# Optimization experiments

Measured on AMD Instinct MI355X. Metric: run time of the kernel, lower is better.

The kernel has to match this reference:

```python
import jax, jax.numpy as jnp
import numpy as np

B, T, QD, CD = 64, 1024, 1024, 512  # batch, encoder steps, query_dim, context_dim


def setup_inputs() -> dict:
    key = jax.random.key(0)
    k1, k2, k3, k4 = jax.random.split(key, 4)
    query = jax.random.normal(k1, (B, 1, QD), dtype=jnp.float32)
    inputs = jax.random.normal(k2, (B, T, CD), dtype=jnp.float32)
    # init_states: alpha = [1, 1e-7, 1e-7, ...], u = 0.5, sq = 1.4
    alpha = jnp.concatenate([jnp.ones((B, 1)), jnp.full((B, T - 1), 1e-7)], axis=1).astype(jnp.float32)
    u = jnp.full((B, 1), 0.5, dtype=jnp.float32)
    sq = jnp.full((B, 1), 1.4, dtype=jnp.float32)
    W_u = (jax.random.normal(k3, (QD + CD, 1)) * 0.02).astype(jnp.float32)
    b_u = jnp.zeros((1,), dtype=jnp.float32)
    W_sq = (jax.random.normal(k4, (QD + CD, 1)) * 0.02).astype(jnp.float32)
    b_sq = jnp.zeros((1,), dtype=jnp.float32)
    return {"query": query, "inputs": inputs, "alpha": alpha, "u": u, "sq": sq,
            "W_u": W_u, "b_u": b_u, "W_sq": W_sq, "b_sq": b_sq}


def reference(query, inputs, alpha, u, sq, W_u, b_u, W_sq, b_sq):
    # shift alpha forward by one step (pad a zero at position 0)
    fwd_shifted = jnp.pad(alpha[:, :-1], ((0, 0), (1, 0)))            # [B, T]
    a = ((1.0 - u) * alpha + u * fwd_shifted + 1e-6) ** sq           # [B, T]
    a = a / jnp.sum(a, axis=1, keepdims=True)                        # normalized alpha
    context = jnp.einsum('bt,btc->bc', a, inputs)                    # [B, CD]
    ta_input = jnp.concatenate([context, query[:, 0, :]], axis=-1)   # [B, CD+QD]
    u_new = jax.nn.sigmoid(ta_input @ W_u + b_u)                     # [B, 1]
    sq_new = jax.nn.sigmoid(ta_input @ W_sq + b_sq) + 1.0            # [B, 1] (dynamicsq)
    return context, a, u_new, sq_new
```

## Files before the change

kernel.cpp:

```cpp
#include <hip/hip_runtime.h>
#include <math.h>

#define B_  64
#define T_  1024
#define QD_ 1024
#define CD_ 512

__global__ __launch_bounds__(256) void attn_alpha_kernel(
    const float* __restrict__ alpha, const float* __restrict__ u,
    const float* __restrict__ sq, float* __restrict__ out_a)
{
    const int b   = blockIdx.x;
    const int tid = threadIdx.x;
    __shared__ float s_alpha[T_];
    __shared__ float s_red[4];

    ((float4*)s_alpha)[tid] = ((const float4*)(alpha + (size_t)b * T_))[tid];
    __syncthreads();

    const float ub  = u[b];
    const float sqb = sq[b];
    const float omu = 1.0f - ub;

    const int t0 = tid * 4;
    float raw[4];
    float lsum = 0.f;
#pragma unroll
    for (int i = 0; i < 4; ++i) {
        const int t = t0 + i;
        const float prev = (t == 0) ? 0.f : s_alpha[t - 1];
        const float x = omu * s_alpha[t] + ub * prev + 1e-6f;
        const float r = powf(x, sqb);
        raw[i] = r;
        lsum += r;
    }
#pragma unroll
    for (int off = 32; off > 0; off >>= 1) lsum += __shfl_down(lsum, off);
    if ((tid & 63) == 0) s_red[tid >> 6] = lsum;
    __syncthreads();
    if (tid == 0) s_red[0] = s_red[0] + s_red[1] + s_red[2] + s_red[3];
    __syncthreads();
    const float inv = 1.0f / s_red[0];

    float4 o;
    o.x = raw[0] * inv; o.y = raw[1] * inv; o.z = raw[2] * inv; o.w = raw[3] * inv;
    ((float4*)(out_a + (size_t)b * T_))[tid] = o;
}

__global__ __launch_bounds__(128) void attn_ctx_partial(
    const float* __restrict__ inputs, const float* __restrict__ a,
    float* __restrict__ part, int S, int seg_len)
{
    const int seg = blockIdx.x;
    const int b   = blockIdx.y;
    const int tid = threadIdx.x;

    __shared__ float s_a[T_];
    const float* ab = a + (size_t)b * T_ + (size_t)seg * seg_len;
    for (int i = tid; i < seg_len; i += 128) s_a[i] = ab[i];
    __syncthreads();

    const float4* in4 =
        (const float4*)(inputs + ((size_t)b * T_ + (size_t)seg * seg_len) * CD_);

    float4 acc = {0.f, 0.f, 0.f, 0.f};
#pragma unroll 8
    for (int i = 0; i < seg_len; ++i) {
        const float av = s_a[i];
        const float4 x = in4[(size_t)i * 128 + tid];
        acc.x += av * x.x; acc.y += av * x.y; acc.z += av * x.z; acc.w += av * x.w;
    }
    ((float4*)(part + ((size_t)b * S + seg) * CD_))[tid] = acc;
}

__global__ __launch_bounds__(128) void attn_ctx_atomic(
    const float* __restrict__ inputs, const float* __restrict__ a,
    float* __restrict__ ctx, int S, int seg_len)
{
    const int seg = blockIdx.x;
    const int b   = blockIdx.y;
    const int tid = threadIdx.x;

    __shared__ float s_a[T_];
    const float* ab = a + (size_t)b * T_ + (size_t)seg * seg_len;
    for (int i = tid; i < seg_len; i += 128) s_a[i] = ab[i];
    __syncthreads();

    const float4* in4 =
        (const float4*)(inputs + ((size_t)b * T_ + (size_t)seg * seg_len) * CD_);

    float4 acc = {0.f, 0.f, 0.f, 0.f};
#pragma unroll 8
    for (int i = 0; i < seg_len; ++i) {
        const float av = s_a[i];
        const float4 x = in4[(size_t)i * 128 + tid];
        acc.x += av * x.x; acc.y += av * x.y; acc.z += av * x.z; acc.w += av * x.w;
    }
    float* dst = ctx + (size_t)b * CD_ + tid * 4;
    atomicAdd(dst + 0, acc.x);
    atomicAdd(dst + 1, acc.y);
    atomicAdd(dst + 2, acc.z);
    atomicAdd(dst + 3, acc.w);
}

__global__ __launch_bounds__(512) void attn_final(
    const float* __restrict__ part, int S,
    const float* __restrict__ query,
    const float* __restrict__ W_u, const float* __restrict__ b_u,
    const float* __restrict__ W_sq, const float* __restrict__ b_sq,
    float* __restrict__ out_ctx, float* __restrict__ out_u,
    float* __restrict__ out_sq, int use_ws)
{
    const int b   = blockIdx.x;
    const int tid = threadIdx.x;

    float c;
    if (use_ws) {
        c = 0.f;
        for (int s = 0; s < S; ++s)
            c += part[((size_t)b * S + s) * CD_ + tid];
        out_ctx[(size_t)b * CD_ + tid] = c;
    } else {
        c = out_ctx[(size_t)b * CD_ + tid];
    }

    const float* qb = query + (size_t)b * QD_;
    const float q0 = qb[tid];
    const float q1 = qb[tid + 512];

    float du = c * W_u[tid]  + q0 * W_u[512 + tid]  + q1 * W_u[1024 + tid];
    float ds = c * W_sq[tid] + q0 * W_sq[512 + tid] + q1 * W_sq[1024 + tid];

#pragma unroll
    for (int off = 32; off > 0; off >>= 1) {
        du += __shfl_down(du, off);
        ds += __shfl_down(ds, off);
    }
    __shared__ float s_u[8], s_s[8];
    if ((tid & 63) == 0) { s_u[tid >> 6] = du; s_s[tid >> 6] = ds; }
    __syncthreads();
    if (tid == 0) {
        float su = 0.f, ss = 0.f;
#pragma unroll
        for (int w = 0; w < 8; ++w) { su += s_u[w]; ss += s_s[w]; }
        su += b_u[0];
        ss += b_sq[0];
        out_u[b]  = 1.0f / (1.0f + expf(-su));
        out_sq[b] = 1.0f / (1.0f + expf(-ss)) + 1.0f;
    }
}

extern "C" void kernel_launch(void* const* d_in, const int* in_sizes, int n_in,
                              void* d_out, int out_size, void* d_ws, size_t ws_size,
                              hipStream_t stream) {
    const float* query  = (const float*)d_in[0];
    const float* inputs = (const float*)d_in[1];
    const float* alpha  = (const float*)d_in[2];
    const float* u      = (const float*)d_in[3];
    const float* sq     = (const float*)d_in[4];
    const float* W_u    = (const float*)d_in[5];
    const float* b_u    = (const float*)d_in[6];
    const float* W_sq   = (const float*)d_in[7];
    const float* b_sq   = (const float*)d_in[8];

    float* out      = (float*)d_out;
    float* out_ctx  = out;
    float* out_a    = out + (size_t)B_ * CD_;
    float* out_u    = out_a + (size_t)B_ * T_;
    float* out_sq   = out_u + B_;

    attn_alpha_kernel<<<B_, 256, 0, stream>>>(alpha, u, sq, out_a);

    int S = 32;
    while (S > 1 && ws_size < (size_t)B_ * S * CD_ * sizeof(float)) S >>= 1;
    const int use_ws = (ws_size >= (size_t)B_ * S * CD_ * sizeof(float)) ? 1 : 0;
    const int seg_len = T_ / S;
    float* part = (float*)d_ws;

    if (use_ws) {
        attn_ctx_partial<<<dim3(S, B_), 128, 0, stream>>>(inputs, out_a, part, S, seg_len);
    } else {
        hipMemsetAsync(out_ctx, 0, (size_t)B_ * CD_ * sizeof(float), stream);
        attn_ctx_atomic<<<dim3(S, B_), 128, 0, stream>>>(inputs, out_a, out_ctx, S, seg_len);
    }

    attn_final<<<B_, 512, 0, stream>>>(part, S, query, W_u, b_u, W_sq, b_sq,
                                       out_ctx, out_u, out_sq, use_ws);
}
```

Baseline: 221.5 us.

## Fuse context reduction and gating heads into partial kernel via last-block counter

The separate final kernel is removed. Each batch's segment blocks write their partial context, then bump a per-batch atomic counter, and the last block to arrive sums the partials and computes the u/sq sigmoid heads. This saves one kernel launch and its dependency gap, at the cost of a memset for the counters, extra threadfences, and a serial tail run by a single 128-thread block per batch. The alpha kernel also switches to the fast __powf/__expf intrinsics, which trades some accuracy.

```diff
diff --git a/kernel.cpp b/kernel.cpp
--- a/kernel.cpp
+++ b/kernel.cpp
@@ -30,7 +30,7 @@
         const int t = t0 + i;
         const float prev = (t == 0) ? 0.f : s_alpha[t - 1];
         const float x = omu * s_alpha[t] + ub * prev + 1e-6f;
-        const float r = powf(x, sqb);
+        const float r = __powf(x, sqb);
         raw[i] = r;
         lsum += r;
     }
@@ -47,9 +47,84 @@
     ((float4*)(out_a + (size_t)b * T_))[tid] = o;
 }
 
-__global__ __launch_bounds__(128) void attn_ctx_partial(
+template <int SEG>
+__global__ __launch_bounds__(128) void attn_ctx_fused(
     const float* __restrict__ inputs, const float* __restrict__ a,
-    float* __restrict__ part, int S, int seg_len)
+    const float* __restrict__ query,
+    const float* __restrict__ W_u, const float* __restrict__ b_u,
+    const float* __restrict__ W_sq, const float* __restrict__ b_sq,
+    float* __restrict__ part, unsigned int* __restrict__ cnt,
+    float* __restrict__ out_ctx, float* __restrict__ out_u,
+    float* __restrict__ out_sq)
+{
+    constexpr int SLEN = T_ / SEG;
+    const int seg = blockIdx.x;
+    const int b   = blockIdx.y;
+    const int tid = threadIdx.x;
+
+    __shared__ float s_a[SLEN];
+    if (tid < SLEN) s_a[tid] = a[(size_t)b * T_ + seg * SLEN + tid];
+    __syncthreads();
+
+    const float4* in4 =
+        (const float4*)(inputs + ((size_t)b * T_ + (size_t)seg * SLEN) * CD_);
+
+    float4 acc = {0.f, 0.f, 0.f, 0.f};
+#pragma unroll 8
+    for (int i = 0; i < SLEN; ++i) {
+        const float av = s_a[i];
+        const float4 x = in4[(size_t)i * 128 + tid];
+        acc.x += av * x.x; acc.y += av * x.y; acc.z += av * x.z; acc.w += av * x.w;
+    }
+    ((float4*)(part + ((size_t)b * SEG + seg) * CD_))[tid] = acc;
+
+    __threadfence();
+    __syncthreads();
+    __shared__ unsigned int s_old;
+    if (tid == 0) s_old = atomicAdd(&cnt[b], 1u);
+    __syncthreads();
+    if (s_old != SEG - 1) return;
+    __threadfence();
+
+    float4 c = {0.f, 0.f, 0.f, 0.f};
+    const float4* p4 = (const float4*)(part + (size_t)b * SEG * CD_);
+#pragma unroll 8
+    for (int s = 0; s < SEG; ++s) {
+        const float4 x = p4[(size_t)s * 128 + tid];
+        c.x += x.x; c.y += x.y; c.z += x.z; c.w += x.w;
+    }
+    ((float4*)(out_ctx + (size_t)b * CD_))[tid] = c;
+
+    const float* qb = query + (size_t)b * QD_;
+    const int ch = tid * 4;
+    float du = c.x * W_u[ch]  + c.y * W_u[ch + 1]  + c.z * W_u[ch + 2]  + c.w * W_u[ch + 3];
+    float ds = c.x * W_sq[ch] + c.y * W_sq[ch + 1] + c.z * W_sq[ch + 2] + c.w * W_sq[ch + 3];
+#pragma unroll
+    for (int j = 0; j < QD_ / 128; ++j) {
+        const int q_idx = j * 128 + tid;
+        const float q = qb[q_idx];
+        du += q * W_u[CD_ + q_idx];
+        ds += q * W_sq[CD_ + q_idx];
+    }
+#pragma unroll
+    for (int off = 32; off > 0; off >>= 1) {
+        du += __shfl_down(du, off);
+        ds += __shfl_down(ds, off);
+    }
+    __shared__ float s_u[2], s_s[2];
+    if ((tid & 63) == 0) { s_u[tid >> 6] = du; s_s[tid >> 6] = ds; }
+    __syncthreads();
+    if (tid == 0) {
+        const float su = s_u[0] + s_u[1] + b_u[0];
+        const float ss = s_s[0] + s_s[1] + b_sq[0];
+        out_u[b]  = 1.0f / (1.0f + __expf(-su));
+        out_sq[b] = 1.0f / (1.0f + __expf(-ss)) + 1.0f;
+    }
+}
+
+__global__ __launch_bounds__(128) void attn_ctx_atomic(
+    const float* __restrict__ inputs, const float* __restrict__ a,
+    float* __restrict__ ctx, int S, int seg_len)
 {
     const int seg = blockIdx.x;
     const int b   = blockIdx.y;
@@ -64,33 +139,6 @@
         (const float4*)(inputs + ((size_t)b * T_ + (size_t)seg * seg_len) * CD_);
 
     float4 acc = {0.f, 0.f, 0.f, 0.f};
-#pragma unroll 8
-    for (int i = 0; i < seg_len; ++i) {
-        const float av = s_a[i];
-        const float4 x = in4[(size_t)i * 128 + tid];
-        acc.x += av * x.x; acc.y += av * x.y; acc.z += av * x.z; acc.w += av * x.w;
-    }
-    ((float4*)(part + ((size_t)b * S + seg) * CD_))[tid] = acc;
-}
-
-__global__ __launch_bounds__(128) void attn_ctx_atomic(
-    const float* __restrict__ inputs, const float* __restrict__ a,
-    float* __restrict__ ctx, int S, int seg_len)
-{
-    const int seg = blockIdx.x;
-    const int b   = blockIdx.y;
-    const int tid = threadIdx.x;
-
-    __shared__ float s_a[T_];
-    const float* ab = a + (size_t)b * T_ + (size_t)seg * seg_len;
-    for (int i = tid; i < seg_len; i += 128) s_a[i] = ab[i];
-    __syncthreads();
-
-    const float4* in4 =
-        (const float4*)(inputs + ((size_t)b * T_ + (size_t)seg * seg_len) * CD_);
-
-    float4 acc = {0.f, 0.f, 0.f, 0.f};
-#pragma unroll 8
     for (int i = 0; i < seg_len; ++i) {
         const float av = s_a[i];
         const float4 x = in4[(size_t)i * 128 + tid];
@@ -103,34 +151,23 @@
     atomicAdd(dst + 3, acc.w);
 }
 
-__global__ __launch_bounds__(512) void attn_final(
-    const float* __restrict__ part, int S,
+__global__ __launch_bounds__(512) void attn_heads(
     const float* __restrict__ query,
     const float* __restrict__ W_u, const float* __restrict__ b_u,
     const float* __restrict__ W_sq, const float* __restrict__ b_sq,
-    float* __restrict__ out_ctx, float* __restrict__ out_u,
-    float* __restrict__ out_sq, int use_ws)
+    const float* __restrict__ out_ctx, float* __restrict__ out_u,
+    float* __restrict__ out_sq)
 {
     const int b   = blockIdx.x;
     const int tid = threadIdx.x;
 
-    float c;
-    if (use_ws) {
-        c = 0.f;
-        for (int s = 0; s < S; ++s)
-            c += part[((size_t)b * S + s) * CD_ + tid];
-        out_ctx[(size_t)b * CD_ + tid] = c;
-    } else {
-        c = out_ctx[(size_t)b * CD_ + tid];
-    }
-
+    const float c  = out_ctx[(size_t)b * CD_ + tid];
     const float* qb = query + (size_t)b * QD_;
     const float q0 = qb[tid];
     const float q1 = qb[tid + 512];
 
     float du = c * W_u[tid]  + q0 * W_u[512 + tid]  + q1 * W_u[1024 + tid];
     float ds = c * W_sq[tid] + q0 * W_sq[512 + tid] + q1 * W_sq[1024 + tid];
-
 #pragma unroll
     for (int off = 32; off > 0; off >>= 1) {
         du += __shfl_down(du, off);
@@ -140,13 +177,11 @@
     if ((tid & 63) == 0) { s_u[tid >> 6] = du; s_s[tid >> 6] = ds; }
     __syncthreads();
     if (tid == 0) {
-        float su = 0.f, ss = 0.f;
+        float su = b_u[0], ss = b_sq[0];
 #pragma unroll
         for (int w = 0; w < 8; ++w) { su += s_u[w]; ss += s_s[w]; }
-        su += b_u[0];
-        ss += b_sq[0];
-        out_u[b]  = 1.0f / (1.0f + expf(-su));
-        out_sq[b] = 1.0f / (1.0f + expf(-ss)) + 1.0f;
+        out_u[b]  = 1.0f / (1.0f + __expf(-su));
+        out_sq[b] = 1.0f / (1.0f + __expf(-ss)) + 1.0f;
     }
 }
 
@@ -171,19 +206,21 @@
 
     attn_alpha_kernel<<<B_, 256, 0, stream>>>(alpha, u, sq, out_a);
 
-    int S = 32;
-    while (S > 1 && ws_size < (size_t)B_ * S * CD_ * sizeof(float)) S >>= 1;
-    const int use_ws = (ws_size >= (size_t)B_ * S * CD_ * sizeof(float)) ? 1 : 0;
-    const int seg_len = T_ / S;
-    float* part = (float*)d_ws;
-
-    if (use_ws) {
-        attn_ctx_partial<<<dim3(S, B_), 128, 0, stream>>>(inputs, out_a, part, S, seg_len);
+    constexpr int SEG = 32;
+    const size_t part_bytes = (size_t)B_ * SEG * CD_ * sizeof(float);
+    const size_t cnt_bytes  = (size_t)B_ * sizeof(unsigned int);
+
+    if (ws_size >= part_bytes + cnt_bytes) {
+        float* part        = (float*)d_ws;
+        unsigned int* cnt  = (unsigned int*)((char*)d_ws + part_bytes);
+        hipMemsetAsync(cnt, 0, cnt_bytes, stream);
+        attn_ctx_fused<SEG><<<dim3(SEG, B_), 128, 0, stream>>>(
+            inputs, out_a, query, W_u, b_u, W_sq, b_sq,
+            part, cnt, out_ctx, out_u, out_sq);
     } else {
         hipMemsetAsync(out_ctx, 0, (size_t)B_ * CD_ * sizeof(float), stream);
-        attn_ctx_atomic<<<dim3(S, B_), 128, 0, stream>>>(inputs, out_a, out_ctx, S, seg_len);
-    }
-
-    attn_final<<<B_, 512, 0, stream>>>(part, S, query, W_u, b_u, W_sq, b_sq,
-                                       out_ctx, out_u, out_sq, use_ws);
-}
+        attn_ctx_atomic<<<dim3(SEG, B_), 128, 0, stream>>>(inputs, out_a, out_ctx, SEG, T_ / SEG);
+        attn_heads<<<B_, 512, 0, stream>>>(query, W_u, b_u, W_sq, b_sq,
+                                           out_ctx, out_u, out_sq);
+    }
+}
```

After: 409.2 us. +84.8%, slower.
